# Optimization experiments

Measured on AMD Instinct MI355X. Metric: run time of the kernel, lower is better.

Reference implementation:

```python
import jax, jax.numpy as jnp
import numpy as np

N_NODES = 100000
N_EDGES = 1600000
IN_F = 32
D = 128
OUT = 16


def setup_inputs() -> dict:
    key = jax.random.key(0)
    ks = jax.random.split(key, 12)
    inp = {
        "x": jax.random.normal(ks[0], (N_NODES, IN_F), dtype=jnp.float32),
        "edge_index": jax.random.randint(ks[1], (2, N_EDGES), 0, N_NODES, dtype=jnp.int64),
        # node embedder (Linear IN_F -> D)
        "W_emb": jax.random.normal(ks[2], (IN_F, D), dtype=jnp.float32) / np.sqrt(IN_F),
        "b_emb": jnp.zeros((D,), dtype=jnp.float32),
        # conv1: relation weight, root weight, bias
        "W1_rel": jax.random.normal(ks[3], (D, D), dtype=jnp.float32) / np.sqrt(D),
        "W1_root": jax.random.normal(ks[4], (D, D), dtype=jnp.float32) / np.sqrt(D),
        "b1": jnp.zeros((D,), dtype=jnp.float32),
        # conv2
        "W2_rel": jax.random.normal(ks[5], (D, D), dtype=jnp.float32) / np.sqrt(D),
        "W2_root": jax.random.normal(ks[6], (D, D), dtype=jnp.float32) / np.sqrt(D),
        "b2": jnp.zeros((D,), dtype=jnp.float32),
        # final layer D -> OUT
        "W_out": jax.random.normal(ks[7], (D, OUT), dtype=jnp.float32) / np.sqrt(D),
        "b_out": jnp.zeros((OUT,), dtype=jnp.float32),
    }
    return inp


def _rgcn_mean(h, src, dst, W_rel, W_root, b):
    # FastRGCNConv with num_relations=1, aggr='mean':
    # out_i = mean_{j -> i}(h_j @ W_rel) + h_i @ W_root + b
    msg = h[src] @ W_rel  # [E, D] gather + per-edge transform
    agg = jax.ops.segment_sum(msg, dst, num_segments=N_NODES)
    cnt = jax.ops.segment_sum(jnp.ones((dst.shape[0],), dtype=h.dtype), dst,
                              num_segments=N_NODES)
    agg = agg / jnp.maximum(cnt, 1.0)[:, None]  # scatter-mean; isolated nodes -> 0
    return agg + h @ W_root + b


def reference(x, edge_index, W_emb, b_emb, W1_rel, W1_root, b1,
              W2_rel, W2_root, b2, W_out, b_out):
    src, dst = edge_index[0], edge_index[1]
    h = x @ W_emb + b_emb                                   # node embed
    h = jax.nn.relu(_rgcn_mean(h, src, dst, W1_rel, W1_root, b1))
    h = jax.nn.relu(_rgcn_mean(h, src, dst, W2_rel, W2_root, b2))
    return h @ W_out + b_out                                # [N_NODES, OUT]
```

## Files before the change

### kernel.cpp

```cpp
#include <hip/hip_runtime.h>
#include <hip/hip_bf16.h>

#define N_NODES 100000
#define N_EDGES 1600000
#define IN_F    32
#define D       128
#define OUT_F   16
#define NB      ((N_NODES + 255) / 256)
#define NSLICE  8
#define SLICE_NODES (N_NODES / NSLICE)

#define NI4     (N_EDGES / 4)
#define EBLK    ((NI4 + 1023) / 1024)
#define NCNT    (NSLICE * EBLK)

typedef __attribute__((ext_vector_type(8))) short  bf16x8;
typedef __attribute__((ext_vector_type(4))) float  f32x4;

__device__ __forceinline__ unsigned short f2bf(float x) {
    unsigned u = __float_as_uint(x);
    unsigned r = (u + 0x7FFFu + ((u >> 16) & 1u)) >> 16;
    return (unsigned short)r;
}
__device__ __forceinline__ float bf2f(unsigned short h) {
    return __uint_as_float(((unsigned)h) << 16);
}

__global__ __launch_bounds__(256) void k_embed(const float* __restrict__ x,
                                               const float* __restrict__ W,
                                               const float* __restrict__ b,
                                               unsigned short* __restrict__ h_hi,
                                               unsigned short* __restrict__ h_lo) {
    __shared__ float xs[16][IN_F];
    const int base = blockIdx.x * 16;

    if (threadIdx.x < 128) {
        int r = threadIdx.x >> 3, c4 = (threadIdx.x & 7) << 2;
        *reinterpret_cast<float4*>(&xs[r][c4]) =
            *reinterpret_cast<const float4*>(x + (long)(base + r) * IN_F + c4);
    }
    __syncthreads();

    const int nl   = threadIdx.x >> 4;
    const int col0 = (threadIdx.x & 15) << 3;

    float acc[8];
    {
        float4 b0 = *reinterpret_cast<const float4*>(b + col0);
        float4 b1 = *reinterpret_cast<const float4*>(b + col0 + 4);
        acc[0] = b0.x; acc[1] = b0.y; acc[2] = b0.z; acc[3] = b0.w;
        acc[4] = b1.x; acc[5] = b1.y; acc[6] = b1.z; acc[7] = b1.w;
    }
#pragma unroll
    for (int k = 0; k < IN_F; ++k) {
        const float xv = xs[nl][k];
        float4 w0 = *reinterpret_cast<const float4*>(W + k * D + col0);
        float4 w1 = *reinterpret_cast<const float4*>(W + k * D + col0 + 4);
        acc[0] += xv * w0.x; acc[1] += xv * w0.y; acc[2] += xv * w0.z; acc[3] += xv * w0.w;
        acc[4] += xv * w1.x; acc[5] += xv * w1.y; acc[6] += xv * w1.z; acc[7] += xv * w1.w;
    }

    unsigned short hh[8], ll[8];
#pragma unroll
    for (int j = 0; j < 8; ++j) {
        unsigned short h = f2bf(acc[j]);
        hh[j] = h;
        ll[j] = f2bf(acc[j] - bf2f(h));
    }
    long off = (long)(base + nl) * D + col0;
    *reinterpret_cast<bf16x8*>(h_hi + off) = *reinterpret_cast<bf16x8*>(hh);
    *reinterpret_cast<bf16x8*>(h_lo + off) = *reinterpret_cast<bf16x8*>(ll);
}

__global__ __launch_bounds__(256) void k_count(const int* __restrict__ dst,
                                               int* __restrict__ cnt) {
    const int slice = blockIdx.x & (NSLICE - 1);
    const int chunk = blockIdx.x >> 3;
    const int lo = slice * SLICE_NODES;
    const int hi = lo + SLICE_NODES;
    const int4* dst4 = reinterpret_cast<const int4*>(dst);
    const int i4base = chunk * 1024;
    const int tid = threadIdx.x;

    int4 d[4];
    bool ok[4];
#pragma unroll
    for (int j = 0; j < 4; ++j) {
        int idx = i4base + j * 256 + tid;
        ok[j] = idx < NI4;
        if (ok[j]) d[j] = dst4[idx];
    }
#pragma unroll
    for (int j = 0; j < 4; ++j) {
        if (ok[j]) {
            if (d[j].x >= lo && d[j].x < hi) atomicAdd(&cnt[d[j].x], 1);
            if (d[j].y >= lo && d[j].y < hi) atomicAdd(&cnt[d[j].y], 1);
            if (d[j].z >= lo && d[j].z < hi) atomicAdd(&cnt[d[j].z], 1);
            if (d[j].w >= lo && d[j].w < hi) atomicAdd(&cnt[d[j].w], 1);
        }
    }
}

__global__ __launch_bounds__(256) void k_scan1(const int* __restrict__ cnt,
                                               int* __restrict__ part,
                                               int* __restrict__ blockSums) {
    __shared__ int s[256];
    int i = blockIdx.x * 256 + threadIdx.x;
    int v = (i < N_NODES) ? cnt[i] : 0;
    s[threadIdx.x] = v;
    __syncthreads();
    for (int off = 1; off < 256; off <<= 1) {
        int x = (threadIdx.x >= off) ? s[threadIdx.x - off] : 0;
        __syncthreads();
        s[threadIdx.x] += x;
        __syncthreads();
    }
    if (i < N_NODES) part[i] = s[threadIdx.x] - v;
    if (threadIdx.x == 255) blockSums[blockIdx.x] = s[255];
}

__global__ __launch_bounds__(512) void k_scan2(int* __restrict__ blockSums) {
    __shared__ int s[512];
    int t = threadIdx.x;
    int v = (t < NB) ? blockSums[t] : 0;
    s[t] = v;
    __syncthreads();
    for (int off = 1; off < 512; off <<= 1) {
        int x = (t >= off) ? s[t - off] : 0;
        __syncthreads();
        s[t] += x;
        __syncthreads();
    }
    if (t < NB) blockSums[t] = s[t] - v;
}

__global__ __launch_bounds__(256) void k_scan3(int* __restrict__ offsets,
                                               const int* __restrict__ blockSums,
                                               int* __restrict__ cursor) {
    int i = blockIdx.x * 256 + threadIdx.x;
    if (i < N_NODES) {
        int o = offsets[i] + blockSums[blockIdx.x];
        offsets[i] = o;
        cursor[i]  = o;
    }
}

__global__ __launch_bounds__(256) void k_fill(const int* __restrict__ src,
                                              const int* __restrict__ dst,
                                              int* __restrict__ cursor,
                                              int* __restrict__ csr) {
    const int slice = blockIdx.x & (NSLICE - 1);
    const int chunk = blockIdx.x >> 3;
    const int lo = slice * SLICE_NODES;
    const int hi = lo + SLICE_NODES;
    const int4* dst4 = reinterpret_cast<const int4*>(dst);
    const int4* src4 = reinterpret_cast<const int4*>(src);
    const int i4base = chunk * 1024;
    const int tid = threadIdx.x;

    int4 d[4], s[4];
    bool ok[4];
#pragma unroll
    for (int j = 0; j < 4; ++j) {
        int idx = i4base + j * 256 + tid;
        ok[j] = idx < NI4;
        if (ok[j]) { d[j] = dst4[idx]; s[j] = src4[idx]; }
    }
#pragma unroll
    for (int j = 0; j < 4; ++j) {
        if (ok[j]) {
            if (d[j].x >= lo && d[j].x < hi) { int p = atomicAdd(&cursor[d[j].x], 1); csr[p] = s[j].x; }
            if (d[j].y >= lo && d[j].y < hi) { int p = atomicAdd(&cursor[d[j].y], 1); csr[p] = s[j].y; }
            if (d[j].z >= lo && d[j].z < hi) { int p = atomicAdd(&cursor[d[j].z], 1); csr[p] = s[j].z; }
            if (d[j].w >= lo && d[j].w < hi) { int p = atomicAdd(&cursor[d[j].w], 1); csr[p] = s[j].w; }
        }
    }
}

__global__ __launch_bounds__(256) void k_wprep(const float* __restrict__ W1r,
                                               const float* __restrict__ W1o,
                                               const float* __restrict__ W2r,
                                               const float* __restrict__ W2o,
                                               unsigned short* __restrict__ wp) {
    int c = blockIdx.x * 256 + threadIdx.x;
    int layer = c >> 12;
    int ko = (c >> 7) & 31;
    int n = c & 127;
    const float* Wrel  = layer ? W2r : W1r;
    const float* Wroot = layer ? W2o : W1o;

    unsigned short hi[8], lo[8];
#pragma unroll
    for (int j = 0; j < 8; ++j) {
        int k = ko * 8 + j;
        float w = (k < D) ? Wrel[k * D + n] : Wroot[(k - D) * D + n];
        unsigned short h = f2bf(w);
        hi[j] = h;
        lo[j] = f2bf(w - bf2f(h));
    }
    unsigned short* base = wp + layer * 65536 + ((ko * 128 + n) << 3);
    *reinterpret_cast<bf16x8*>(base)         = *reinterpret_cast<bf16x8*>(hi);
    *reinterpret_cast<bf16x8*>(base + 32768) = *reinterpret_cast<bf16x8*>(lo);
}

template <bool LAST>
__global__ __launch_bounds__(512) void k_fused(const unsigned short* __restrict__ hin_hi,
                                               const unsigned short* __restrict__ hin_lo,
                                               const int* __restrict__ csr,
                                               const int* __restrict__ offsets,
                                               const int* __restrict__ cnt,
                                               const unsigned short* __restrict__ Wh,
                                               const unsigned short* __restrict__ Wl,
                                               const float* __restrict__ b,
                                               unsigned short* __restrict__ ho_hi,
                                               unsigned short* __restrict__ ho_lo,
                                               const float* __restrict__ Wout,
                                               const float* __restrict__ bout,
                                               float* __restrict__ outp) {
    __shared__ unsigned short Ahi[32 * 32 * 8];
    __shared__ unsigned short Alo[32 * 32 * 8];
    const int base = blockIdx.x * 32;
    const int tid  = threadIdx.x;

    {
        const int ko  = tid & 15;
        const int q8  = ko << 3;
        const int row = tid >> 4;
        const int node = base + row;
        const int beg = offsets[node];
        const int deg = cnt[node];
        const int end = beg + deg;

        float a0[8], a1[8];
#pragma unroll
        for (int j = 0; j < 8; ++j) { a0[j] = 0.f; a1[j] = 0.f; }

        int i = beg;
        for (; i + 3 < end; i += 4) {
            int s0 = csr[i], s1 = csr[i + 1], s2 = csr[i + 2], s3 = csr[i + 3];
            bf16x8 v0 = *reinterpret_cast<const bf16x8*>(hin_hi + (long)s0 * D + q8);
            bf16x8 v1 = *reinterpret_cast<const bf16x8*>(hin_hi + (long)s1 * D + q8);
            bf16x8 v2 = *reinterpret_cast<const bf16x8*>(hin_hi + (long)s2 * D + q8);
            bf16x8 v3 = *reinterpret_cast<const bf16x8*>(hin_hi + (long)s3 * D + q8);
#pragma unroll
            for (int j = 0; j < 8; ++j) {
                a0[j] += bf2f((unsigned short)v0[j]) + bf2f((unsigned short)v1[j]);
                a1[j] += bf2f((unsigned short)v2[j]) + bf2f((unsigned short)v3[j]);
            }
        }
        for (; i < end; ++i) {
            int s0 = csr[i];
            bf16x8 v0 = *reinterpret_cast<const bf16x8*>(hin_hi + (long)s0 * D + q8);
#pragma unroll
            for (int j = 0; j < 8; ++j) a0[j] += bf2f((unsigned short)v0[j]);
        }

        const float sc = 1.f / fmaxf((float)deg, 1.f);
        unsigned short hh[8], ll[8];
#pragma unroll
        for (int j = 0; j < 8; ++j) {
            float v = (a0[j] + a1[j]) * sc;
            unsigned short h = f2bf(v);
            hh[j] = h;
            ll[j] = f2bf(v - bf2f(h));
        }
        const int byteoff = ((ko * 32 + row) * 16) ^ ((ko & 7) << 4);
        *reinterpret_cast<bf16x8*>(reinterpret_cast<char*>(Ahi) + byteoff) =
            *reinterpret_cast<bf16x8*>(hh);
        *reinterpret_cast<bf16x8*>(reinterpret_cast<char*>(Alo) + byteoff) =
            *reinterpret_cast<bf16x8*>(ll);
    }

    {
        int ko16 = tid & 15;
        int row  = tid >> 4;
        long off = (long)(base + row) * D + ko16 * 8;
        bf16x8 vh = *reinterpret_cast<const bf16x8*>(hin_hi + off);
        bf16x8 vl = *reinterpret_cast<const bf16x8*>(hin_lo + off);
        int ko = 16 + ko16;
        int byteoff = ((ko * 32 + row) * 16) ^ ((ko & 7) << 4);
        *reinterpret_cast<bf16x8*>(reinterpret_cast<char*>(Ahi) + byteoff) = vh;
        *reinterpret_cast<bf16x8*>(reinterpret_cast<char*>(Alo) + byteoff) = vl;
    }
    __syncthreads();

    const int lane = tid & 63;
    const int wid  = tid >> 6;
    const int mw  = wid & 1;
    const int nwq = wid >> 1;
    const int l15 = lane & 15;
    const int l4  = lane >> 4;

    f32x4 acc[2];
#pragma unroll
    for (int ct = 0; ct < 2; ++ct) acc[ct] = (f32x4){0.f, 0.f, 0.f, 0.f};

    const int arow = mw * 16 + l15;

#pragma unroll
    for (int s = 0; s < 8; ++s) {
        const int ks = s * 4 + l4;
        const int abyte = ((ks * 32 + arow) * 16) ^ ((ks & 7) << 4);
        bf16x8 ah = *reinterpret_cast<const bf16x8*>(
                        reinterpret_cast<const char*>(Ahi) + abyte);
        bf16x8 al = *reinterpret_cast<const bf16x8*>(
                        reinterpret_cast<const char*>(Alo) + abyte);
#pragma unroll
        for (int ct = 0; ct < 2; ++ct) {
            const int colb = nwq * 32 + ct * 16 + l15;
            const long bidx = ((long)(ks * 128 + colb)) << 3;
            bf16x8 bh = *reinterpret_cast<const bf16x8*>(Wh + bidx);
            bf16x8 bl = *reinterpret_cast<const bf16x8*>(Wl + bidx);
            acc[ct] = __builtin_amdgcn_mfma_f32_16x16x32_bf16(ah, bh, acc[ct], 0, 0, 0);
            acc[ct] = __builtin_amdgcn_mfma_f32_16x16x32_bf16(al, bh, acc[ct], 0, 0, 0);
            acc[ct] = __builtin_amdgcn_mfma_f32_16x16x32_bf16(ah, bl, acc[ct], 0, 0, 0);
        }
    }

    if (!LAST) {
#pragma unroll
        for (int ct = 0; ct < 2; ++ct) {
            const int col = nwq * 32 + ct * 16 + l15;
            const float bv = b[col];
#pragma unroll
            for (int r = 0; r < 4; ++r) {
                long node = base + mw * 16 + l4 * 4 + r;
                float v = fmaxf(acc[ct][r] + bv, 0.f);
                unsigned short h = f2bf(v);
                ho_hi[node * D + col] = h;
                ho_lo[node * D + col] = f2bf(v - bf2f(h));
            }
        }
    } else {
        __syncthreads();
        float* hsm = reinterpret_cast<float*>(Ahi);
#pragma unroll
        for (int ct = 0; ct < 2; ++ct) {
            const int col = nwq * 32 + ct * 16 + l15;
            const float bv = b[col];
#pragma unroll
            for (int r = 0; r < 4; ++r) {
                int nl = mw * 16 + l4 * 4 + r;
                hsm[nl * D + ((col + 4 * nl) & 127)] = fmaxf(acc[ct][r] + bv, 0.f);
            }
        }
        __syncthreads();

        const int nl = tid >> 4;
        const int oo = tid & 15;
        float acc0 = bout[oo];
#pragma unroll 8
        for (int k = 0; k < D; ++k) {
            float hv = hsm[nl * D + ((k + 4 * nl) & 127)];
            acc0 += hv * Wout[k * OUT_F + oo];
        }
        outp[(long)(base + nl) * OUT_F + oo] = acc0;
    }
}

extern "C" void kernel_launch(void* const* d_in, const int* in_sizes, int n_in,
                              void* d_out, int out_size, void* d_ws, size_t ws_size,
                              hipStream_t stream) {
    const float* x      = (const float*)d_in[0];
    const int*   edge   = (const int*)d_in[1];
    const float* W_emb  = (const float*)d_in[2];
    const float* b_emb  = (const float*)d_in[3];
    const float* W1_rel = (const float*)d_in[4];
    const float* W1_root= (const float*)d_in[5];
    const float* b1     = (const float*)d_in[6];
    const float* W2_rel = (const float*)d_in[7];
    const float* W2_root= (const float*)d_in[8];
    const float* b2     = (const float*)d_in[9];
    const float* W_out  = (const float*)d_in[10];
    const float* b_out  = (const float*)d_in[11];
    float* out = (float*)d_out;

    const int* src = edge;
    const int* dst = edge + N_EDGES;

    const size_t ND = (size_t)N_NODES * D;

    unsigned short* hA_hi = (unsigned short*)d_ws;
    unsigned short* hA_lo = hA_hi + ND;
    unsigned short* hB_hi = hA_lo + ND;
    unsigned short* hB_lo = hB_hi + ND;
    int*   cnt     = (int*)(hB_lo + ND);
    int*   offsets = cnt + N_NODES;
    int*   cursor  = offsets + N_NODES;
    int*   bsums   = cursor + N_NODES;
    unsigned short* wpack = (unsigned short*)(bsums + 400);
    int*   csr     = (int*)(wpack + 4 * 32768);

    hipMemsetAsync(cnt, 0, N_NODES * sizeof(int), stream);
    k_count<<<NCNT, 256, 0, stream>>>(dst, cnt);
    k_scan1<<<NB, 256, 0, stream>>>(cnt, offsets, bsums);
    k_scan2<<<1, 512, 0, stream>>>(bsums);
    k_scan3<<<NB, 256, 0, stream>>>(offsets, bsums, cursor);
    k_fill<<<NCNT, 256, 0, stream>>>(src, dst, cursor, csr);
    k_wprep<<<32, 256, 0, stream>>>(W1_rel, W1_root, W2_rel, W2_root, wpack);

    k_embed<<<N_NODES / 16, 256, 0, stream>>>(x, W_emb, b_emb, hA_hi, hA_lo);

    k_fused<false><<<N_NODES / 32, 512, 0, stream>>>(
        hA_hi, hA_lo, csr, offsets, cnt,
        wpack, wpack + 32768, b1, hB_hi, hB_lo, nullptr, nullptr, nullptr);

    k_fused<true><<<N_NODES / 32, 512, 0, stream>>>(
        hB_hi, hB_lo, csr, offsets, cnt,
        wpack + 65536, wpack + 98304, b2, nullptr, nullptr, W_out, b_out, out);
}
```

Before: 467.7 us.

## Sort nodes by in-degree so fused blocks process nodes with similar degree

Builds a degree histogram during the scan, counting-sorts the nodes by descending in-degree (capped at 127) into a permutation, and has both fused conv kernels process nodes in that order. Grouping nodes of similar degree in one block is meant to reduce load imbalance and wave divergence in the per-node neighbour gather loop. In exchange it adds two small kernels, scattered root-feature reads and output writes through the permutation, and loses the locality of contiguous node ranges.

```diff
diff --git a/kernel.cpp b/kernel.cpp
--- a/kernel.cpp
+++ b/kernel.cpp
@@ -103,12 +103,16 @@
 
 __global__ __launch_bounds__(256) void k_scan1(const int* __restrict__ cnt,
                                                int* __restrict__ part,
-                                               int* __restrict__ blockSums) {
+                                               int* __restrict__ blockSums,
+                                               int* __restrict__ hist) {
     __shared__ int s[256];
+    __shared__ int lh[128];
+    if (threadIdx.x < 128) lh[threadIdx.x] = 0;
     int i = blockIdx.x * 256 + threadIdx.x;
     int v = (i < N_NODES) ? cnt[i] : 0;
     s[threadIdx.x] = v;
     __syncthreads();
+    if (i < N_NODES) atomicAdd(&lh[min(v, 127)], 1);
     for (int off = 1; off < 256; off <<= 1) {
         int x = (threadIdx.x >= off) ? s[threadIdx.x - off] : 0;
         __syncthreads();
@@ -117,6 +121,9 @@
     }
     if (i < N_NODES) part[i] = s[threadIdx.x] - v;
     if (threadIdx.x == 255) blockSums[blockIdx.x] = s[255];
+    __syncthreads();
+    if (threadIdx.x < 128 && lh[threadIdx.x] > 0)
+        atomicAdd(&hist[threadIdx.x], lh[threadIdx.x]);
 }
 
 __global__ __launch_bounds__(512) void k_scan2(int* __restrict__ blockSums) {
@@ -143,6 +150,44 @@
         offsets[i] = o;
         cursor[i]  = o;
     }
+}
+
+__global__ __launch_bounds__(128) void k_binscan(const int* __restrict__ hist,
+                                                 int* __restrict__ binCursor) {
+    __shared__ int s[128];
+    int t = threadIdx.x;
+    int rev = 127 - t;
+    int v = hist[rev];
+    s[t] = v;
+    __syncthreads();
+    for (int off = 1; off < 128; off <<= 1) {
+        int x = (t >= off) ? s[t - off] : 0;
+        __syncthreads();
+        s[t] += x;
+        __syncthreads();
+    }
+    binCursor[rev] = s[t] - v;
+}
+
+__global__ __launch_bounds__(256) void k_permfill(const int* __restrict__ cnt,
+                                                  int* __restrict__ binCursor,
+                                                  int* __restrict__ perm) {
+    __shared__ int lhist[128], lbase[128];
+    const int tid = threadIdx.x;
+    if (tid < 128) lhist[tid] = 0;
+    __syncthreads();
+    int node = blockIdx.x * 256 + tid;
+    int d = 0, myloc = 0;
+    bool ok = node < N_NODES;
+    if (ok) {
+        d = min(cnt[node], 127);
+        myloc = atomicAdd(&lhist[d], 1);
+    }
+    __syncthreads();
+    if (tid < 128 && lhist[tid] > 0)
+        lbase[tid] = atomicAdd(&binCursor[tid], lhist[tid]);
+    __syncthreads();
+    if (ok) perm[lbase[d] + myloc] = node;
 }
 
 __global__ __launch_bounds__(256) void k_fill(const int* __restrict__ src,
@@ -209,6 +254,7 @@
                                                const int* __restrict__ csr,
                                                const int* __restrict__ offsets,
                                                const int* __restrict__ cnt,
+                                               const int* __restrict__ perm,
                                                const unsigned short* __restrict__ Wh,
                                                const unsigned short* __restrict__ Wl,
                                                const float* __restrict__ b,
@@ -226,7 +272,7 @@
         const int ko  = tid & 15;
         const int q8  = ko << 3;
         const int row = tid >> 4;
-        const int node = base + row;
+        const int node = perm[base + row];
         const int beg = offsets[node];
         const int deg = cnt[node];
         const int end = beg + deg;
@@ -274,7 +320,7 @@
     {
         int ko16 = tid & 15;
         int row  = tid >> 4;
-        long off = (long)(base + row) * D + ko16 * 8;
+        long off = (long)perm[base + row] * D + ko16 * 8;
         bf16x8 vh = *reinterpret_cast<const bf16x8*>(hin_hi + off);
         bf16x8 vl = *reinterpret_cast<const bf16x8*>(hin_lo + off);
         int ko = 16 + ko16;
@@ -324,7 +370,7 @@
             const float bv = b[col];
 #pragma unroll
             for (int r = 0; r < 4; ++r) {
-                long node = base + mw * 16 + l4 * 4 + r;
+                long node = perm[base + mw * 16 + l4 * 4 + r];
                 float v = fmaxf(acc[ct][r] + bv, 0.f);
                 unsigned short h = f2bf(v);
                 ho_hi[node * D + col] = h;
@@ -354,7 +400,7 @@
             float hv = hsm[nl * D + ((k + 4 * nl) & 127)];
             acc0 += hv * Wout[k * OUT_F + oo];
         }
-        outp[(long)(base + nl) * OUT_F + oo] = acc0;
+        outp[(long)perm[base + nl] * OUT_F + oo] = acc0;
     }
 }
 
@@ -385,27 +431,32 @@
     unsigned short* hB_hi = hA_lo + ND;
     unsigned short* hB_lo = hB_hi + ND;
     int*   cnt     = (int*)(hB_lo + ND);
-    int*   offsets = cnt + N_NODES;
+    int*   hist    = cnt + N_NODES;
+    int*   offsets = hist + 128;
     int*   cursor  = offsets + N_NODES;
     int*   bsums   = cursor + N_NODES;
-    unsigned short* wpack = (unsigned short*)(bsums + 400);
+    int*   binCur  = bsums + 400;
+    int*   perm    = binCur + 128;
+    unsigned short* wpack = (unsigned short*)(perm + N_NODES);
     int*   csr     = (int*)(wpack + 4 * 32768);
 
-    hipMemsetAsync(cnt, 0, N_NODES * sizeof(int), stream);
+    hipMemsetAsync(cnt, 0, (N_NODES + 128) * sizeof(int), stream);
     k_count<<<NCNT, 256, 0, stream>>>(dst, cnt);
-    k_scan1<<<NB, 256, 0, stream>>>(cnt, offsets, bsums);
+    k_scan1<<<NB, 256, 0, stream>>>(cnt, offsets, bsums, hist);
     k_scan2<<<1, 512, 0, stream>>>(bsums);
     k_scan3<<<NB, 256, 0, stream>>>(offsets, bsums, cursor);
+    k_binscan<<<1, 128, 0, stream>>>(hist, binCur);
+    k_permfill<<<NB, 256, 0, stream>>>(cnt, binCur, perm);
     k_fill<<<NCNT, 256, 0, stream>>>(src, dst, cursor, csr);
     k_wprep<<<32, 256, 0, stream>>>(W1_rel, W1_root, W2_rel, W2_root, wpack);
 
     k_embed<<<N_NODES / 16, 256, 0, stream>>>(x, W_emb, b_emb, hA_hi, hA_lo);
 
     k_fused<false><<<N_NODES / 32, 512, 0, stream>>>(
-        hA_hi, hA_lo, csr, offsets, cnt,
+        hA_hi, hA_lo, csr, offsets, cnt, perm,
         wpack, wpack + 32768, b1, hB_hi, hB_lo, nullptr, nullptr, nullptr);
 
     k_fused<true><<<N_NODES / 32, 512, 0, stream>>>(
-        hB_hi, hB_lo, csr, offsets, cnt,
+        hB_hi, hB_lo, csr, offsets, cnt, perm,
         wpack + 65536, wpack + 98304, b2, nullptr, nullptr, W_out, b_out, out);
 }
```

After: 480.4 us. 2.7% more time.
